# Optimization experiments

Measured on AMD Instinct MI355X. Metric: run time of the kernel, lower is better.

The kernel has to match this reference:

```python
import jax, jax.numpy as jnp
import numpy as np

NUM_TOKENS = 1024  # codebook size (n_embed)
CODE_DIM = 256     # embedding_dim
BETA = 0.25


def setup_inputs() -> dict:
    key = jax.random.key(0)
    k1, k2 = jax.random.split(key)
    z = jax.random.normal(k1, (64, 512, CODE_DIM), dtype=jnp.float32)
    weight = jax.random.normal(k2, (NUM_TOKENS, CODE_DIM), dtype=jnp.float32)
    return {"z": z, "weight": weight}


def reference(z, weight):
    # z: [B, T, D]; weight: [K, D]
    z_flat = z.reshape(-1, CODE_DIM)                       # [N, D]
    # squared euclidean distances: ||z||^2 + ||w||^2 - 2 z.w
    d = (jnp.sum(z_flat ** 2, axis=1, keepdims=True)
         + jnp.sum(weight ** 2, axis=1)
         - 2.0 * jnp.matmul(z_flat, weight.T))             # [N, K]
    min_encoding_indices = jnp.argmin(d, axis=1)           # [N]
    z_q = weight[min_encoding_indices].reshape(z.shape)    # gather

    # perplexity from mean one-hot usage (avoid materializing one-hot via bincount)
    counts = jnp.bincount(min_encoding_indices, length=NUM_TOKENS)
    e_mean = counts.astype(z.dtype) / z_flat.shape[0]
    perplexity = jnp.exp(-jnp.sum(e_mean * jnp.log(e_mean + 1e-10)))

    # commitment loss (codebook is EMA-updated, so z_q is detached)
    loss = BETA * jnp.mean((jax.lax.stop_gradient(z_q) - z) ** 2)
    # straight-through estimator
    z_q_st = z + jax.lax.stop_gradient(z_q - z)
    return (loss, z_q_st, min_encoding_indices, perplexity)
```

## Files before the change

kernel.cpp:

```cpp
#include <hip/hip_runtime.h>

#define N_TOKENS 32768
#define K_CODES  1024
#define DIM      256
#define BETA     0.25f

typedef unsigned long long u64;
typedef _Float16 half8 __attribute__((ext_vector_type(8)));
typedef float floatx4 __attribute__((ext_vector_type(4)));

__global__ void init_kernel(const float* __restrict__ w, float* __restrict__ wn,
                            int* __restrict__ counts, u64* __restrict__ keys,
                            _Float16* __restrict__ whiG, _Float16* __restrict__ wloG) {
    int k = blockIdx.x;
    int lane = threadIdx.x;
    float4 v = *(const float4*)(w + (size_t)k * DIM + lane * 4);
    float vals[4] = {v.x, v.y, v.z, v.w};
    float s = 0.f;
    #pragma unroll
    for (int e = 0; e < 4; e++) {
        s += vals[e] * vals[e];
        _Float16 h = (_Float16)vals[e];
        whiG[k * DIM + lane * 4 + e] = h;
        wloG[k * DIM + lane * 4 + e] = (_Float16)(vals[e] - (float)h);
    }
    #pragma unroll
    for (int off = 32; off; off >>= 1) s += __shfl_down(s, off);
    if (lane == 0) { wn[k] = s; counts[k] = 0; }
    if (lane < 32) keys[k * 32 + lane] = ~0ull;
}

__global__ __launch_bounds__(256, 2) void argmin_kernel(
    const float* __restrict__ z, const _Float16* __restrict__ whiG,
    const _Float16* __restrict__ wloG, const float* __restrict__ wn,
    u64* __restrict__ keys)
{
    constexpr int ZS = 40;
    __shared__ _Float16 zhi[128 * ZS], zlo[128 * ZS];
    __shared__ _Float16 whi[256 * ZS], wlo[256 * ZS];
    __shared__ float wns[256];

    const int tid  = threadIdx.x;
    const int lane = tid & 63;
    const int wid  = tid >> 6;
    const int wm   = wid >> 1;
    const int wq   = wid & 1;
    const int t_   = blockIdx.x & 255;
    const int q    = blockIdx.x >> 8;
    const int tok0  = t_ * 128;
    const int kbase = q * 256;

    wns[tid] = wn[kbase + tid];

    floatx4 acc[4][8];
    #pragma unroll
    for (int i = 0; i < 4; i++)
        #pragma unroll
        for (int j = 0; j < 8; j++)
            acc[i][j] = (floatx4){0.f, 0.f, 0.f, 0.f};

    const int r0 = tid >> 2;
    const int g0 = tid & 3;

    for (int dt = 0; dt < 8; ++dt) {
        const int d0 = dt * 32;
        __syncthreads();

        #pragma unroll
        for (int s = 0; s < 2; s++) {
            int t = r0 + s * 64;
            const float* p = z + (size_t)(tok0 + t) * DIM + d0 + g0 * 8;
            float4 a = *(const float4*)p;
            float4 b = *(const float4*)(p + 4);
            float vals[8] = {a.x, a.y, a.z, a.w, b.x, b.y, b.z, b.w};
            half8 hv, lv;
            #pragma unroll
            for (int e = 0; e < 8; e++) {
                _Float16 h = (_Float16)vals[e];
                hv[e] = h;
                lv[e] = (_Float16)(vals[e] - (float)h);
            }
            *(half8*)&zhi[t * ZS + g0 * 8] = hv;
            *(half8*)&zlo[t * ZS + g0 * 8] = lv;
        }
        #pragma unroll
        for (int s = 0; s < 4; s++) {
            int t = r0 + s * 64;
            size_t goff = (size_t)(kbase + t) * DIM + d0 + g0 * 8;
            *(half8*)&whi[t * ZS + g0 * 8] = *(const half8*)&whiG[goff];
            *(half8*)&wlo[t * ZS + g0 * 8] = *(const half8*)&wloG[goff];
        }
        __syncthreads();

        const int koff = (lane >> 4) * 8;
        half8 ah[4], al[4];
        #pragma unroll
        for (int i = 0; i < 4; i++) {
            int off = (wm * 64 + i * 16 + (lane & 15)) * ZS + koff;
            ah[i] = *(const half8*)&zhi[off];
            al[i] = *(const half8*)&zlo[off];
        }
        #pragma unroll
        for (int j = 0; j < 8; j++) {
            int off = (wq * 128 + j * 16 + (lane & 15)) * ZS + koff;
            half8 bh = *(const half8*)&whi[off];
            half8 bl = *(const half8*)&wlo[off];
            #pragma unroll
            for (int i = 0; i < 4; i++) {
                acc[i][j] = __builtin_amdgcn_mfma_f32_16x16x32_f16(ah[i], bh, acc[i][j], 0, 0, 0);
                acc[i][j] = __builtin_amdgcn_mfma_f32_16x16x32_f16(ah[i], bl, acc[i][j], 0, 0, 0);
                acc[i][j] = __builtin_amdgcn_mfma_f32_16x16x32_f16(al[i], bh, acc[i][j], 0, 0, 0);
            }
        }
    }

    #pragma unroll
    for (int i = 0; i < 4; i++) {
        #pragma unroll
        for (int r = 0; r < 4; r++) {
            float bv = 3.4e38f; int bi = 0;
            #pragma unroll
            for (int j = 0; j < 8; j++) {
                int cl = wq * 128 + j * 16 + (lane & 15);
                float dist = wns[cl] - 2.0f * acc[i][j][r];
                if (dist < bv) { bv = dist; bi = kbase + cl; }
            }
            unsigned uu = __float_as_uint(bv);
            unsigned ss = (uu & 0x80000000u) ? ~uu : (uu | 0x80000000u);
            u64 key = ((u64)ss << 32) | (unsigned)bi;
            #pragma unroll
            for (int m = 1; m < 16; m <<= 1) {
                u64 o = __shfl_xor(key, m);
                if (o < key) key = o;
            }
            if ((lane & 15) == 0) {
                int token = tok0 + wm * 64 + i * 16 + (lane >> 4) * 4 + r;
                atomicMin(&keys[token], key);
            }
        }
    }
}

__global__ void gather_loss_kernel(const float* __restrict__ z,
                                   const float* __restrict__ w,
                                   const u64* __restrict__ keys,
                                   float* __restrict__ zq_out,
                                   float* __restrict__ idxf,
                                   int* __restrict__ counts,
                                   float* __restrict__ partials)
{
    __shared__ float red[4];
    int tid = threadIdx.x;
    int lane = tid & 63;
    int wid = blockIdx.x * 4 + (tid >> 6);
    float s = 0.0f;
    #pragma unroll
    for (int it = 0; it < 4; it++) {
        int tok = wid + it * 8192;
        u64 key = 0;
        if (lane == 0) key = keys[tok];
        key = __shfl(key, 0);
        int k = (int)(unsigned)(key & 0xFFFFFFFFull);
        float4 wv = *(const float4*)(w + (size_t)k * DIM + lane * 4);
        float4 zv = *(const float4*)(z + (size_t)tok * DIM + lane * 4);
        *(float4*)(zq_out + (size_t)tok * DIM + lane * 4) = wv;
        float dx = wv.x - zv.x, dy = wv.y - zv.y, dz = wv.z - zv.z, dw = wv.w - zv.w;
        s += dx * dx + dy * dy + dz * dz + dw * dw;
        if (lane == 0) {
            idxf[tok] = (float)k;
            atomicAdd(&counts[k], 1);
        }
    }
    #pragma unroll
    for (int off = 32; off; off >>= 1) s += __shfl_down(s, off);
    if (lane == 0) red[tid >> 6] = s;
    __syncthreads();
    if (tid == 0)
        partials[blockIdx.x] = red[0] + red[1] + red[2] + red[3];
}

__global__ void finalize_kernel(const int* __restrict__ counts,
                                const float* __restrict__ partials,
                                float* __restrict__ loss_out,
                                float* __restrict__ ppl_out)
{
    __shared__ float redE[16], redL[16];
    int tid = threadIdx.x;
    float e = (float)counts[tid] * (1.0f / (float)N_TOKENS);
    float t = -e * logf(e + 1e-10f);
    float p = partials[tid] + partials[tid + 1024];
    #pragma unroll
    for (int off = 32; off; off >>= 1) {
        t += __shfl_down(t, off);
        p += __shfl_down(p, off);
    }
    if ((tid & 63) == 0) { redE[tid >> 6] = t; redL[tid >> 6] = p; }
    __syncthreads();
    if (tid == 0) {
        float se = 0.0f, sl = 0.0f;
        #pragma unroll
        for (int i = 0; i < 16; i++) { se += redE[i]; sl += redL[i]; }
        *ppl_out = expf(se);
        *loss_out = BETA * sl / (float)((size_t)N_TOKENS * DIM);
    }
}

extern "C" void kernel_launch(void* const* d_in, const int* in_sizes, int n_in,
                              void* d_out, int out_size, void* d_ws, size_t ws_size,
                              hipStream_t stream) {
    const float* z = (const float*)d_in[0];
    const float* w = (const float*)d_in[1];
    float* out = (float*)d_out;

    float* loss_out = out;
    float* zq_out   = out + 1;
    float* idxf     = out + 1 + (size_t)N_TOKENS * DIM;
    float* ppl_out  = out + (out_size - 1);

    float* wn       = (float*)d_ws;
    int*   counts   = (int*)d_ws + 1024;
    float* partials = (float*)d_ws + 2048;
    u64*   keys     = (u64*)((char*)d_ws + 16384);
    _Float16* whiG  = (_Float16*)((char*)d_ws + 16384 + (size_t)N_TOKENS * 8);
    _Float16* wloG  = whiG + (size_t)K_CODES * DIM;

    init_kernel<<<K_CODES, 64, 0, stream>>>(w, wn, counts, keys, whiG, wloG);
    argmin_kernel<<<4 * 256, 256, 0, stream>>>(z, whiG, wloG, wn, keys);
    gather_loss_kernel<<<2048, 256, 0, stream>>>(z, w, keys, zq_out, idxf, counts, partials);
    finalize_kernel<<<1, 1024, 0, stream>>>(counts, partials, loss_out, ppl_out);
}
```

Measured before the change: 159.1 us.

## Halve argmin code tile, swizzle LDS, raise occupancy, vectorize key loads

Each argmin block now covers 128 codes instead of 256, doubling the grid and halving accumulator registers so three blocks can fit per CU. LDS row padding is replaced by an XOR swizzle to avoid bank conflicts with a smaller footprint, and codebook norms are kept in registers instead of shared memory. The gather kernel loads all four keys per lane directly instead of a lane-0 load plus shuffle. The trade-off is that each z tile is loaded and split into fp16 hi/lo parts twice as often across the grid.

```diff
diff --git a/kernel.cpp b/kernel.cpp
--- a/kernel.cpp
+++ b/kernel.cpp
@@ -8,6 +8,10 @@
 typedef unsigned long long u64;
 typedef _Float16 half8 __attribute__((ext_vector_type(8)));
 typedef float floatx4 __attribute__((ext_vector_type(4)));
+
+__device__ __forceinline__ int gsw(int row, int g) {
+    return g ^ ((row ^ (row >> 2)) & 3);
+}
 
 __global__ void init_kernel(const float* __restrict__ w, float* __restrict__ wn,
                             int* __restrict__ counts, u64* __restrict__ keys,
@@ -30,15 +34,13 @@
     if (lane < 32) keys[k * 32 + lane] = ~0ull;
 }
 
-__global__ __launch_bounds__(256, 2) void argmin_kernel(
+__global__ __launch_bounds__(256, 3) void argmin_kernel(
     const float* __restrict__ z, const _Float16* __restrict__ whiG,
     const _Float16* __restrict__ wloG, const float* __restrict__ wn,
     u64* __restrict__ keys)
 {
-    constexpr int ZS = 40;
-    __shared__ _Float16 zhi[128 * ZS], zlo[128 * ZS];
-    __shared__ _Float16 whi[256 * ZS], wlo[256 * ZS];
-    __shared__ float wns[256];
+    __shared__ _Float16 zhi[128 * 32], zlo[128 * 32];
+    __shared__ _Float16 whi[128 * 32], wlo[128 * 32];
 
     const int tid  = threadIdx.x;
     const int lane = tid & 63;
@@ -48,15 +50,22 @@
     const int t_   = blockIdx.x & 255;
     const int q    = blockIdx.x >> 8;
     const int tok0  = t_ * 128;
-    const int kbase = q * 256;
-
-    wns[tid] = wn[kbase + tid];
-
-    floatx4 acc[4][8];
+    const int kbase = q * 128;
+
+    const int n  = lane & 15;
+    const int kg = lane >> 4;
+    const int ga = kg ^ ((n ^ (n >> 2)) & 3);
+
+    float wnv[4];
+    #pragma unroll
+    for (int j = 0; j < 4; j++)
+        wnv[j] = wn[kbase + wq * 64 + j * 16 + n];
+
+    floatx4 acc[4][4];
     #pragma unroll
     for (int i = 0; i < 4; i++)
         #pragma unroll
-        for (int j = 0; j < 8; j++)
+        for (int j = 0; j < 4; j++)
             acc[i][j] = (floatx4){0.f, 0.f, 0.f, 0.f};
 
     const int r0 = tid >> 2;
@@ -80,29 +89,30 @@
                 hv[e] = h;
                 lv[e] = (_Float16)(vals[e] - (float)h);
             }
-            *(half8*)&zhi[t * ZS + g0 * 8] = hv;
-            *(half8*)&zlo[t * ZS + g0 * 8] = lv;
-        }
-        #pragma unroll
-        for (int s = 0; s < 4; s++) {
+            int off = t * 32 + gsw(t, g0) * 8;
+            *(half8*)&zhi[off] = hv;
+            *(half8*)&zlo[off] = lv;
+        }
+        #pragma unroll
+        for (int s = 0; s < 2; s++) {
             int t = r0 + s * 64;
             size_t goff = (size_t)(kbase + t) * DIM + d0 + g0 * 8;
-            *(half8*)&whi[t * ZS + g0 * 8] = *(const half8*)&whiG[goff];
-            *(half8*)&wlo[t * ZS + g0 * 8] = *(const half8*)&wloG[goff];
+            int off = t * 32 + gsw(t, g0) * 8;
+            *(half8*)&whi[off] = *(const half8*)&whiG[goff];
+            *(half8*)&wlo[off] = *(const half8*)&wloG[goff];
         }
         __syncthreads();
 
-        const int koff = (lane >> 4) * 8;
         half8 ah[4], al[4];
         #pragma unroll
         for (int i = 0; i < 4; i++) {
-            int off = (wm * 64 + i * 16 + (lane & 15)) * ZS + koff;
+            int off = (wm * 64 + i * 16 + n) * 32 + ga * 8;
             ah[i] = *(const half8*)&zhi[off];
             al[i] = *(const half8*)&zlo[off];
         }
         #pragma unroll
-        for (int j = 0; j < 8; j++) {
-            int off = (wq * 128 + j * 16 + (lane & 15)) * ZS + koff;
+        for (int j = 0; j < 4; j++) {
+            int off = (wq * 64 + j * 16 + n) * 32 + ga * 8;
             half8 bh = *(const half8*)&whi[off];
             half8 bl = *(const half8*)&wlo[off];
             #pragma unroll
@@ -120,10 +130,9 @@
         for (int r = 0; r < 4; r++) {
             float bv = 3.4e38f; int bi = 0;
             #pragma unroll
-            for (int j = 0; j < 8; j++) {
-                int cl = wq * 128 + j * 16 + (lane & 15);
-                float dist = wns[cl] - 2.0f * acc[i][j][r];
-                if (dist < bv) { bv = dist; bi = kbase + cl; }
+            for (int j = 0; j < 4; j++) {
+                float dist = wnv[j] - 2.0f * acc[i][j][r];
+                if (dist < bv) { bv = dist; bi = kbase + wq * 64 + j * 16 + n; }
             }
             unsigned uu = __float_as_uint(bv);
             unsigned ss = (uu & 0x80000000u) ? ~uu : (uu | 0x80000000u);
@@ -133,8 +142,8 @@
                 u64 o = __shfl_xor(key, m);
                 if (o < key) key = o;
             }
-            if ((lane & 15) == 0) {
-                int token = tok0 + wm * 64 + i * 16 + (lane >> 4) * 4 + r;
+            if (n == 0) {
+                int token = tok0 + wm * 64 + i * 16 + kg * 4 + r;
                 atomicMin(&keys[token], key);
             }
         }
@@ -153,14 +162,15 @@
     int tid = threadIdx.x;
     int lane = tid & 63;
     int wid = blockIdx.x * 4 + (tid >> 6);
+    u64 k4[4];
+    #pragma unroll
+    for (int it = 0; it < 4; it++)
+        k4[it] = keys[wid + it * 8192];
     float s = 0.0f;
     #pragma unroll
     for (int it = 0; it < 4; it++) {
         int tok = wid + it * 8192;
-        u64 key = 0;
-        if (lane == 0) key = keys[tok];
-        key = __shfl(key, 0);
-        int k = (int)(unsigned)(key & 0xFFFFFFFFull);
+        int k = (int)(unsigned)(k4[it] & 0xFFFFFFFFull);
         float4 wv = *(const float4*)(w + (size_t)k * DIM + lane * 4);
         float4 zv = *(const float4*)(z + (size_t)tok * DIM + lane * 4);
         *(float4*)(zq_out + (size_t)tok * DIM + lane * 4) = wv;
@@ -225,7 +235,7 @@
     _Float16* wloG  = whiG + (size_t)K_CODES * DIM;
 
     init_kernel<<<K_CODES, 64, 0, stream>>>(w, wn, counts, keys, whiG, wloG);
-    argmin_kernel<<<4 * 256, 256, 0, stream>>>(z, whiG, wloG, wn, keys);
+    argmin_kernel<<<8 * 256, 256, 0, stream>>>(z, whiG, wloG, wn, keys);
     gather_loss_kernel<<<2048, 256, 0, stream>>>(z, w, keys, zq_out, idxf, counts, partials);
     finalize_kernel<<<1, 1024, 0, stream>>>(counts, partials, loss_out, ppl_out);
 }
```

Measured after the change: 164.1 us. +3.1%, slower.
